# Optimization experiments

Measured on AMD Instinct MI355X. Metric: run time of the kernel, lower is better.

The kernel has to match this reference:

```python
import jax, jax.numpy as jnp
import numpy as np

B, W_DIM, CIN, COUT, K, H = 16, 512, 512, 512, 3, 64
PAD = (K - 1) // 2          # conv padding, also filtered_lrelu padding
GAIN = float(np.sqrt(2.0))  # lrelu gain (not torgb)
SLOPE = 0.2                 # lrelu slope (not torgb)
CLAMP = 256.0               # conv_clamp
AFFINE_WG = float(1.0 / np.sqrt(W_DIM))  # FullyConnectedLayer weight_gain


def setup_inputs() -> dict:
    key = jax.random.key(0)
    k0, k1, k2, k3 = jax.random.split(key, 4)
    return {
        "x": jax.random.normal(k0, (B, CIN, H, H), jnp.float32),
        "w": jax.random.normal(k1, (B, W_DIM), jnp.float32),
        "affine_weight": jax.random.normal(k2, (CIN, W_DIM), jnp.float32),
        "affine_bias": jnp.ones((CIN,), jnp.float32),       # bias_init=1
        "conv_weight": jax.random.normal(k3, (COUT, CIN, K, K), jnp.float32),
        "bias": jnp.zeros((COUT,), jnp.float32),
        "magnitude_ema": jnp.ones((), jnp.float32),
    }


def reference(x, w, affine_weight, affine_bias, conv_weight, bias, magnitude_ema):
    input_gain = jax.lax.rsqrt(magnitude_ema)
    # --- affine (FullyConnectedLayer, linear act, lr_mult=1) ---
    s = w @ (affine_weight * AFFINE_WG).T + affine_bias          # [B, CIN]
    # --- modulated_conv2d with demodulation (is_torgb=False) ---
    wk = conv_weight * jax.lax.rsqrt(
        jnp.mean(jnp.square(conv_weight), axis=(1, 2, 3), keepdims=True))
    s = s * jax.lax.rsqrt(jnp.mean(jnp.square(s)))
    wb = wk[None] * s[:, None, :, None, None]                    # [B,COUT,CIN,K,K]
    dcoefs = jax.lax.rsqrt(jnp.sum(jnp.square(wb), axis=(2, 3, 4)) + 1e-8)  # [B,COUT]
    wb = wb * dcoefs[:, :, None, None, None] * input_gain
    # grouped conv: groups = batch, one weight set per sample
    xg = x.reshape(1, B * CIN, H, H)
    wg = wb.reshape(B * COUT, CIN, K, K)
    y = jax.lax.conv_general_dilated(
        xg, wg, window_strides=(1, 1), padding=[(PAD, PAD), (PAD, PAD)],
        dimension_numbers=("NCHW", "OIHW", "NCHW"), feature_group_count=B)
    y = y.reshape(B, COUT, H, H)
    # --- filtered_lrelu: up=down=1, fu=fd=None (identity FIR) ---
    # => bias add, zero-pad by `padding`, lrelu * gain, clamp
    y = y + bias[:, None, None]
    y = jnp.pad(y, ((0, 0), (0, 0), (PAD, PAD), (PAD, PAD)))
    y = jnp.where(y >= 0, y, y * SLOPE) * GAIN
    y = jnp.clip(y, -CLAMP, CLAMP)                               # [B,COUT,66,66]
    return y
```

## Files before the change

### kernel.cpp

```cpp
#include <hip/hip_runtime.h>

#define B_     16
#define WDIM   512
#define CIN_   512
#define COUT_  512
#define HH     64
#define KC     32
#define NCHUNK (CIN_/KC)
#define AFFINE_WG 0.044194173824159216f
#define GAIN_  1.4142135623730951f
#define CLAMP_ 256.0f

#define WBYTES 36864
#define XBYTES 42240

typedef __attribute__((ext_vector_type(4))) float f32x4;
typedef __attribute__((ext_vector_type(8))) short bf16x8;
typedef __attribute__((ext_vector_type(8))) unsigned short u16x8;

__device__ __forceinline__ unsigned short f2bf(float f) {
    union { float f; unsigned u; } un; un.f = f;
    unsigned u = un.u;
    u += 0x7FFFu + ((u >> 16) & 1u);
    return (unsigned short)(u >> 16);
}

__device__ __forceinline__ void gl_lds16(const void* g, void* l) {
    __builtin_amdgcn_global_load_lds(
        reinterpret_cast<const __attribute__((address_space(1))) unsigned int*>(
            reinterpret_cast<uintptr_t>(g)),
        reinterpret_cast<__attribute__((address_space(3))) unsigned int*>(
            reinterpret_cast<uintptr_t>(l)),
        16, 0, 0);
}


__global__ void k_affine(const float* __restrict__ w, const float* __restrict__ aw,
                         const float* __restrict__ ab, float* __restrict__ s,
                         float* __restrict__ part) {
    const int tid = threadIdx.x;
    const int b = blockIdx.x >> 1;
    const int c = ((blockIdx.x & 1) << 8) + tid;
    const f32x4* wr = (const f32x4*)(w + (size_t)b * WDIM);
    const f32x4* ar = (const f32x4*)(aw + (size_t)c * WDIM);
    float acc = 0.f;
    #pragma unroll 4
    for (int k = 0; k < WDIM / 4; ++k) {
        f32x4 a = ar[k], bb = wr[k];
        acc += a[0]*bb[0] + a[1]*bb[1] + a[2]*bb[2] + a[3]*bb[3];
    }
    float sv = acc * AFFINE_WG + ab[c];
    s[b * CIN_ + c] = sv;
    __shared__ float red[256];
    red[tid] = sv * sv;
    __syncthreads();
    for (int off = 128; off > 0; off >>= 1) {
        if (tid < off) red[tid] += red[tid + off];
        __syncthreads();
    }
    if (tid == 0) part[blockIdx.x] = red[0];
}

__global__ void k_wnorm(const float* __restrict__ cw, float* __restrict__ alpha,
                        float* __restrict__ Q) {
    const int o = blockIdx.x;
    const int tid = threadIdx.x;
    __shared__ float qsh[512];
    __shared__ float red[256];
    __shared__ float a_sh;
    float tot = 0.f;
    #pragma unroll
    for (int half = 0; half < 2; ++half) {
        const int c = tid + half * 256;
        const float* p = cw + ((size_t)o * 512 + c) * 9;
        float qs = 0.f;
        #pragma unroll
        for (int t = 0; t < 9; ++t) { float v = p[t]; qs += v * v; }
        qsh[c] = qs; tot += qs;
    }
    red[tid] = tot; __syncthreads();
    for (int off = 128; off > 0; off >>= 1) {
        if (tid < off) red[tid] += red[tid + off];
        __syncthreads();
    }
    if (tid == 0) { a_sh = rsqrtf(red[0] * (1.0f / 4608.0f)); alpha[o] = a_sh; }
    __syncthreads();
    const float a2 = a_sh * a_sh;
    Q[(size_t)o * 512 + tid]       = a2 * qsh[tid];
    Q[(size_t)o * 512 + tid + 256] = a2 * qsh[tid + 256];
}

__global__ void k_g(const float* __restrict__ s, const float* __restrict__ part,
                    const float* __restrict__ Q, const float* __restrict__ alpha,
                    const float* __restrict__ ema, float* __restrict__ g) {
    const int tid = threadIdx.x;
    const int b = blockIdx.x >> 1;
    const int o = ((blockIdx.x & 1) << 8) + tid;
    __shared__ float rs2_sh;
    if (tid == 0) {
        float t = 0.f;
        #pragma unroll
        for (int i = 0; i < 32; ++i) t += part[i];
        rs2_sh = 8192.0f / t;
    }
    __syncthreads();
    const f32x4* sh = (const f32x4*)(s + (size_t)b * CIN_);
    const f32x4* qq = (const f32x4*)(Q + (size_t)o * CIN_);
    float d = 0.f;
    #pragma unroll 4
    for (int k = 0; k < CIN_ / 4; ++k) {
        f32x4 a = sh[k], q4 = qq[k];
        d += a[0]*a[0]*q4[0] + a[1]*a[1]*q4[1] + a[2]*a[2]*q4[2] + a[3]*a[3]*q4[3];
    }
    const float ig = rsqrtf(ema[0]);
    g[b * COUT_ + o] = alpha[o] * rsqrtf(d * rs2_sh + 1e-8f) * ig;
}

__global__ void k_wprep2(const float* __restrict__ cw, unsigned short* __restrict__ wb) {
    const int S = blockIdx.x * 256 + threadIdx.x;
    const int p    = S / 2304;
    const int srem = S - p * 2304;
    const int a    = srem * 16;
    const int tap  = a >> 12;
    const int o    = (a >> 6) & 63;
    const int c0   = ((a & 63) ^ ((o & 6) << 3)) >> 1;
    const int ot = p >> 4, cc = p & 15;
    const int og = ot * 64 + o;
    const int cg = cc * 32 + c0;
    const float* src = cw + ((size_t)og * 512 + cg) * 9 + tap;
    u16x8 v;
    #pragma unroll
    for (int j = 0; j < 8; ++j) v[j] = f2bf(src[j * 9]);
    *(u16x8*)(wb + (size_t)S * 8) = v;
}

__global__ void k_xprep2(const float* __restrict__ x, const float* __restrict__ s,
                         const float* __restrict__ part, unsigned short* __restrict__ xbf) {
    __shared__ float rs_sh;
    __shared__ char tile[8 * 4096];
    const int tid = threadIdx.x;
    if (tid == 0) {
        float t = 0.f;
        #pragma unroll
        for (int i = 0; i < 32; ++i) t += part[i];
        rs_sh = rsqrtf(t * (1.0f / 8192.0f));
    }
    __syncthreads();
    const float rs = rs_sh;
    const int blk = blockIdx.x;
    const int b  = blk >> 7;
    const int cc = (blk >> 3) & 15;
    const int rg = blk & 7;
    const int c   = tid >> 3;
    const int k8  = tid & 7;
    const float sc = s[b * CIN_ + cc * 32 + c] * rs;
    const float* src = x + (((size_t)(b * CIN_ + cc * 32 + c)) * HH + rg * 8) * HH + k8 * 8;
    #pragma unroll
    for (int row = 0; row < 8; ++row) {
        const f32x4 v0 = *(const f32x4*)(src + (size_t)row * HH);
        const f32x4 v1 = *(const f32x4*)(src + (size_t)row * HH + 4);
        #pragma unroll
        for (int q = 0; q < 8; ++q) {
            const float v = (q < 4) ? v0[q] : v1[q - 4];
            const int col = k8 * 8 + q + 1;
            const int byte = ((col * 64 + 2 * c) ^ ((col & 6) << 3)) - 64;
            *(unsigned short*)(tile + row * 4096 + byte) = f2bf(v * sc);
        }
    }
    __syncthreads();
    unsigned short* dst = xbf + ((size_t)(b * 16 + cc) * 64 + rg * 8) * 2048;
    const u16x8* tsrc = (const u16x8*)tile;
    #pragma unroll
    for (int k = 0; k < 8; ++k)
        *(u16x8*)(dst + (size_t)(tid + k * 256) * 8) = tsrc[tid + k * 256];
}

__global__ __launch_bounds__(256, 2) void k_conv5(
    const unsigned short* __restrict__ xbf, const unsigned short* __restrict__ wb,
    const float* __restrict__ g, const float* __restrict__ bias,
    float* __restrict__ out) {
    __shared__ char Wl[WBYTES];
    __shared__ char Xl[XBYTES];

    const int tid  = threadIdx.x;
    const int lane = tid & 63;
    const int wv   = tid >> 6;
    const int l15  = lane & 15;
    const int hi   = lane >> 4;

    const int orig = blockIdx.x;
    const int wg = (orig & 7) * 128 + (orig >> 3);
    const int b  = wg >> 6;
    const int ot = (wg >> 3) & 7;
    const int rt = wg & 7;
    const int h0 = rt * 8;

    const f32x4 zero4 = {0.f, 0.f, 0.f, 0.f};
    f32x4 acc[2][4][4];
    #pragma unroll
    for (int rr = 0; rr < 2; ++rr)
        #pragma unroll
        for (int i = 0; i < 4; ++i)
            #pragma unroll
            for (int j = 0; j < 4; ++j) acc[rr][i][j] = zero4;

    {
        unsigned int* x0 = (unsigned int*)Xl;
        for (int i = tid; i < XBYTES / 4; i += 256) x0[i] = 0u;
    }
    __syncthreads();

    const char* wsrc0 = (const char*)wb + (size_t)ot * 16 * WBYTES;
    const char* xsrc0 = (const char*)xbf + (size_t)b * 16 * 262144;

    #pragma unroll 1
    for (int cc = 0; cc < NCHUNK; ++cc) {
        {
            const char* wsrc = wsrc0 + (size_t)cc * WBYTES;
            #pragma unroll
            for (int r = 0; r < 9; ++r)
                gl_lds16(wsrc + r * 4096 + tid * 16, Wl + r * 4096 + tid * 16);
            const char* xsrc = xsrc0 + (size_t)cc * 262144;
            #pragma unroll
            for (int r = 0; r < 10; ++r) {
                const int h_in = h0 - 1 + r;
                if ((unsigned)h_in < 64u)
                    gl_lds16(xsrc + (size_t)h_in * 4096 + tid * 16,
                             Xl + r * 4224 + 64 + tid * 16);
            }
        }
        __syncthreads();

        #pragma unroll
        for (int tap = 0; tap < 9; ++tap) {
            const int ti = tap / 3, tj = tap - ti * 3;
            bf16x8 af[4];
            #pragma unroll
            for (int mi = 0; mi < 4; ++mi) {
                const int o = mi * 16 + l15;
                int byte = (tap << 12) + (o << 6) + (hi << 4);
                byte ^= ((o & 6) << 3);
                af[mi] = *(const bf16x8*)(Wl + byte);
            }
            bf16x8 bg[2][4];
            #pragma unroll
            for (int rr = 0; rr < 2; ++rr) {
                const int row = 2 * wv + rr + ti;
                #pragma unroll
                for (int ni = 0; ni < 4; ++ni) {
                    const int col = ni * 16 + l15 + tj;
                    int byte = (((row * 66 + col) << 5) + (hi << 3)) << 1;
                    byte ^= ((col & 6) << 3);
                    bg[rr][ni] = *(const bf16x8*)(Xl + byte);
                }
            }
            __builtin_amdgcn_s_setprio(1);
            #pragma unroll
            for (int rr = 0; rr < 2; ++rr)
                #pragma unroll
                for (int mi = 0; mi < 4; ++mi)
                    #pragma unroll
                    for (int ni = 0; ni < 4; ++ni)
                        acc[rr][mi][ni] = __builtin_amdgcn_mfma_f32_16x16x32_bf16(
                            af[mi], bg[rr][ni], acc[rr][mi][ni], 0, 0, 0);
            __builtin_amdgcn_s_setprio(0);
        }
        if (cc != NCHUNK - 1) __syncthreads();
    }

    {
        const int obase = ot * 64;
        #pragma unroll
        for (int rr = 0; rr < 2; ++rr) {
            const int orow = h0 + 2 * wv + rr + 1;
            #pragma unroll
            for (int mi = 0; mi < 4; ++mi) {
                #pragma unroll
                for (int r = 0; r < 4; ++r) {
                    const int o = obase + mi * 16 + hi * 4 + r;
                    const float gg = g[b * COUT_ + o];
                    const float bb = bias[o];
                    float* op = out + ((size_t)(b * COUT_ + o) * 66 + orow) * 66;
                    #pragma unroll
                    for (int ni = 0; ni < 4; ++ni) {
                        float v = acc[rr][mi][ni][r] * gg + bb;
                        v = (v >= 0.f ? v : v * 0.2f) * GAIN_;
                        v = fminf(fmaxf(v, -CLAMP_), CLAMP_);
                        op[ni * 16 + l15 + 1] = v;
                    }
                    if (l15 == 0)  op[0]  = 0.f;
                    if (l15 == 15) op[65] = 0.f;
                }
            }
        }
        if (rt == 0 || rt == 7) {
            const int row = (rt == 0) ? 0 : 65;
            for (int i = tid; i < 64 * 66; i += 256) {
                const int o = obase + i / 66, col = i - (i / 66) * 66;
                out[((size_t)(b * COUT_ + o) * 66 + row) * 66 + col] = 0.f;
            }
        }
    }
}

extern "C" void kernel_launch(void* const* d_in, const int* in_sizes, int n_in,
                              void* d_out, int out_size, void* d_ws, size_t ws_size,
                              hipStream_t stream) {
    const float* x    = (const float*)d_in[0];
    const float* w    = (const float*)d_in[1];
    const float* aw   = (const float*)d_in[2];
    const float* ab   = (const float*)d_in[3];
    const float* cw   = (const float*)d_in[4];
    const float* bias = (const float*)d_in[5];
    const float* ema  = (const float*)d_in[6];
    float* out = (float*)d_out;

    float* wsf   = (float*)d_ws;
    float* s     = wsf;
    float* part  = wsf + 8192;
    float* alpha = wsf + 16512;
    float* Q     = wsf + 17024;
    float* g     = wsf + 279168;
    unsigned short* wb  = (unsigned short*)((char*)d_ws + 1179648);
    unsigned short* xbf = (unsigned short*)((char*)d_ws + 5898240);

    k_affine <<<32, 256, 0, stream>>>(w, aw, ab, s, part);
    k_wnorm  <<<512, 256, 0, stream>>>(cw, alpha, Q);
    k_g      <<<32, 256, 0, stream>>>(s, part, Q, alpha, ema, g);
    k_wprep2 <<<1152, 256, 0, stream>>>(cw, wb);
    k_xprep2 <<<2048, 256, 0, stream>>>(x, s, part, xbf);
    k_conv5  <<<1024, 256, 0, stream>>>(xbf, wb, g, bias, out);
}
```

Before: 337.7 us.

## Read conv weights directly from global with prefetch, shrink row tile

The conv kernel stops staging weights in LDS. Each wave now loads its weight fragments straight from global/L2, prefetching the next tap's fragments while the current tap's MFMAs run, and the weight prep drops the LDS XOR swizzle. The row tile is halved to 4 output rows per block, doubling the grid and shrinking LDS so three blocks can fit per CU. In exchange, the same weights are read once per wave instead of once per block, and each block does less compute per x-halo load.

```diff
diff --git a/kernel.cpp b/kernel.cpp
--- a/kernel.cpp
+++ b/kernel.cpp
@@ -12,7 +12,8 @@
 #define CLAMP_ 256.0f
 
 #define WBYTES 36864
-#define XBYTES 42240
+#define XROWB  4224
+#define XBYTES (6 * XROWB)
 
 typedef __attribute__((ext_vector_type(4))) float f32x4;
 typedef __attribute__((ext_vector_type(8))) short bf16x8;
@@ -116,14 +117,14 @@
     g[b * COUT_ + o] = alpha[o] * rsqrtf(d * rs2_sh + 1e-8f) * ig;
 }
 
-__global__ void k_wprep2(const float* __restrict__ cw, unsigned short* __restrict__ wb) {
+__global__ void k_wprep3(const float* __restrict__ cw, unsigned short* __restrict__ wb) {
     const int S = blockIdx.x * 256 + threadIdx.x;
     const int p    = S / 2304;
     const int srem = S - p * 2304;
     const int a    = srem * 16;
     const int tap  = a >> 12;
     const int o    = (a >> 6) & 63;
-    const int c0   = ((a & 63) ^ ((o & 6) << 3)) >> 1;
+    const int c0   = (a & 63) >> 1;
     const int ot = p >> 4, cc = p & 15;
     const int og = ot * 64 + o;
     const int cg = cc * 32 + c0;
@@ -175,11 +176,10 @@
         *(u16x8*)(dst + (size_t)(tid + k * 256) * 8) = tsrc[tid + k * 256];
 }
 
-__global__ __launch_bounds__(256, 2) void k_conv5(
+__global__ __launch_bounds__(256, 3) void k_conv8(
     const unsigned short* __restrict__ xbf, const unsigned short* __restrict__ wb,
     const float* __restrict__ g, const float* __restrict__ bias,
     float* __restrict__ out) {
-    __shared__ char Wl[WBYTES];
     __shared__ char Xl[XBYTES];
 
     const int tid  = threadIdx.x;
@@ -189,20 +189,18 @@
     const int hi   = lane >> 4;
 
     const int orig = blockIdx.x;
-    const int wg = (orig & 7) * 128 + (orig >> 3);
-    const int b  = wg >> 6;
-    const int ot = (wg >> 3) & 7;
-    const int rt = wg & 7;
-    const int h0 = rt * 8;
+    const int wg = (orig & 7) * 256 + (orig >> 3);
+    const int b  = wg >> 7;
+    const int ot = (wg >> 4) & 7;
+    const int rt = wg & 15;
+    const int h0 = rt * 4;
 
     const f32x4 zero4 = {0.f, 0.f, 0.f, 0.f};
-    f32x4 acc[2][4][4];
-    #pragma unroll
-    for (int rr = 0; rr < 2; ++rr)
-        #pragma unroll
-        for (int i = 0; i < 4; ++i)
-            #pragma unroll
-            for (int j = 0; j < 4; ++j) acc[rr][i][j] = zero4;
+    f32x4 acc[4][4];
+    #pragma unroll
+    for (int i = 0; i < 4; ++i)
+        #pragma unroll
+        for (int j = 0; j < 4; ++j) acc[i][j] = zero4;
 
     {
         unsigned int* x0 = (unsigned int*)Xl;
@@ -213,87 +211,83 @@
     const char* wsrc0 = (const char*)wb + (size_t)ot * 16 * WBYTES;
     const char* xsrc0 = (const char*)xbf + (size_t)b * 16 * 262144;
 
+    const int wfo[4] = { (0 * 16 + l15) * 64 + hi * 16, (1 * 16 + l15) * 64 + hi * 16,
+                         (2 * 16 + l15) * 64 + hi * 16, (3 * 16 + l15) * 64 + hi * 16 };
+
     #pragma unroll 1
     for (int cc = 0; cc < NCHUNK; ++cc) {
         {
-            const char* wsrc = wsrc0 + (size_t)cc * WBYTES;
-            #pragma unroll
-            for (int r = 0; r < 9; ++r)
-                gl_lds16(wsrc + r * 4096 + tid * 16, Wl + r * 4096 + tid * 16);
             const char* xsrc = xsrc0 + (size_t)cc * 262144;
             #pragma unroll
-            for (int r = 0; r < 10; ++r) {
+            for (int r = 0; r < 6; ++r) {
                 const int h_in = h0 - 1 + r;
                 if ((unsigned)h_in < 64u)
                     gl_lds16(xsrc + (size_t)h_in * 4096 + tid * 16,
-                             Xl + r * 4224 + 64 + tid * 16);
+                             Xl + r * XROWB + 64 + tid * 16);
             }
         }
         __syncthreads();
 
+        const char* wchunk = wsrc0 + (size_t)cc * WBYTES;
+        bf16x8 afc[4], afn[4];
+        #pragma unroll
+        for (int mi = 0; mi < 4; ++mi)
+            afc[mi] = *(const bf16x8*)(wchunk + wfo[mi]);
         #pragma unroll
         for (int tap = 0; tap < 9; ++tap) {
+            if (tap < 8) {
+                const char* wnext = wchunk + (tap + 1) * 4096;
+                #pragma unroll
+                for (int mi = 0; mi < 4; ++mi)
+                    afn[mi] = *(const bf16x8*)(wnext + wfo[mi]);
+            }
             const int ti = tap / 3, tj = tap - ti * 3;
-            bf16x8 af[4];
-            #pragma unroll
-            for (int mi = 0; mi < 4; ++mi) {
-                const int o = mi * 16 + l15;
-                int byte = (tap << 12) + (o << 6) + (hi << 4);
-                byte ^= ((o & 6) << 3);
-                af[mi] = *(const bf16x8*)(Wl + byte);
-            }
-            bf16x8 bg[2][4];
-            #pragma unroll
-            for (int rr = 0; rr < 2; ++rr) {
-                const int row = 2 * wv + rr + ti;
+            bf16x8 bg[4];
+            const int row = wv + ti;
+            #pragma unroll
+            for (int ni = 0; ni < 4; ++ni) {
+                const int col = ni * 16 + l15 + tj;
+                int byte = (((row * 66 + col) << 5) + (hi << 3)) << 1;
+                byte ^= ((col & 6) << 3);
+                bg[ni] = *(const bf16x8*)(Xl + byte);
+            }
+            __builtin_amdgcn_s_setprio(1);
+            #pragma unroll
+            for (int mi = 0; mi < 4; ++mi)
+                #pragma unroll
+                for (int ni = 0; ni < 4; ++ni)
+                    acc[mi][ni] = __builtin_amdgcn_mfma_f32_16x16x32_bf16(
+                        afc[mi], bg[ni], acc[mi][ni], 0, 0, 0);
+            __builtin_amdgcn_s_setprio(0);
+            #pragma unroll
+            for (int mi = 0; mi < 4; ++mi) afc[mi] = afn[mi];
+        }
+        if (cc != NCHUNK - 1) __syncthreads();
+    }
+
+    {
+        const int obase = ot * 64;
+        const int orow = h0 + wv + 1;
+        #pragma unroll
+        for (int mi = 0; mi < 4; ++mi) {
+            #pragma unroll
+            for (int r = 0; r < 4; ++r) {
+                const int o = obase + mi * 16 + hi * 4 + r;
+                const float gg = g[b * COUT_ + o];
+                const float bb = bias[o];
+                float* op = out + ((size_t)(b * COUT_ + o) * 66 + orow) * 66;
                 #pragma unroll
                 for (int ni = 0; ni < 4; ++ni) {
-                    const int col = ni * 16 + l15 + tj;
-                    int byte = (((row * 66 + col) << 5) + (hi << 3)) << 1;
-                    byte ^= ((col & 6) << 3);
-                    bg[rr][ni] = *(const bf16x8*)(Xl + byte);
+                    float v = acc[mi][ni][r] * gg + bb;
+                    v = (v >= 0.f ? v : v * 0.2f) * GAIN_;
+                    v = fminf(fmaxf(v, -CLAMP_), CLAMP_);
+                    op[ni * 16 + l15 + 1] = v;
                 }
-            }
-            __builtin_amdgcn_s_setprio(1);
-            #pragma unroll
-            for (int rr = 0; rr < 2; ++rr)
-                #pragma unroll
-                for (int mi = 0; mi < 4; ++mi)
-                    #pragma unroll
-                    for (int ni = 0; ni < 4; ++ni)
-                        acc[rr][mi][ni] = __builtin_amdgcn_mfma_f32_16x16x32_bf16(
-                            af[mi], bg[rr][ni], acc[rr][mi][ni], 0, 0, 0);
-            __builtin_amdgcn_s_setprio(0);
-        }
-        if (cc != NCHUNK - 1) __syncthreads();
-    }
-
-    {
-        const int obase = ot * 64;
-        #pragma unroll
-        for (int rr = 0; rr < 2; ++rr) {
-            const int orow = h0 + 2 * wv + rr + 1;
-            #pragma unroll
-            for (int mi = 0; mi < 4; ++mi) {
-                #pragma unroll
-                for (int r = 0; r < 4; ++r) {
-                    const int o = obase + mi * 16 + hi * 4 + r;
-                    const float gg = g[b * COUT_ + o];
-                    const float bb = bias[o];
-                    float* op = out + ((size_t)(b * COUT_ + o) * 66 + orow) * 66;
-                    #pragma unroll
-                    for (int ni = 0; ni < 4; ++ni) {
-                        float v = acc[rr][mi][ni][r] * gg + bb;
-                        v = (v >= 0.f ? v : v * 0.2f) * GAIN_;
-                        v = fminf(fmaxf(v, -CLAMP_), CLAMP_);
-                        op[ni * 16 + l15 + 1] = v;
-                    }
-                    if (l15 == 0)  op[0]  = 0.f;
-                    if (l15 == 15) op[65] = 0.f;
-                }
-            }
-        }
-        if (rt == 0 || rt == 7) {
+                if (l15 == 0)  op[0]  = 0.f;
+                if (l15 == 15) op[65] = 0.f;
+            }
+        }
+        if (rt == 0 || rt == 15) {
             const int row = (rt == 0) ? 0 : 65;
             for (int i = tid; i < 64 * 66; i += 256) {
                 const int o = obase + i / 66, col = i - (i / 66) * 66;
@@ -327,7 +321,7 @@
     k_affine <<<32, 256, 0, stream>>>(w, aw, ab, s, part);
     k_wnorm  <<<512, 256, 0, stream>>>(cw, alpha, Q);
     k_g      <<<32, 256, 0, stream>>>(s, part, Q, alpha, ema, g);
-    k_wprep2 <<<1152, 256, 0, stream>>>(cw, wb);
+    k_wprep3 <<<1152, 256, 0, stream>>>(cw, wb);
     k_xprep2 <<<2048, 256, 0, stream>>>(x, s, part, xbf);
-    k_conv5  <<<1024, 256, 0, stream>>>(xbf, wb, g, bias, out);
-}
+    k_conv8  <<<2048, 256, 0, stream>>>(xbf, wb, g, bias, out);
+}
```

Result: slower. 440.0 us (+30.3%).
